# Optimization experiments

Hardware: AMD Instinct MI355X
Metric: run time of the kernel (lower is better)

The kernel has to match this reference:

```python
import jax, jax.numpy as jnp
import numpy as np

B, N, C = 8, 1024, 768
H, D = 12, 64  # num_heads, head_dim; C == H*D
SCALE = 1.0 / np.sqrt(D)
NEG_INF = -1e9


def setup_inputs() -> dict:
    key = jax.random.key(0)
    k1, k2, k3, k4 = jax.random.split(key, 4)
    x = jax.random.normal(k1, (B, N, C), dtype=jnp.float32)
    # additive padding mask: 0 for valid tokens, -1e9 for padded tail
    lengths = jax.random.randint(k2, (B,), N // 2, N + 1)  # valid lengths per sample
    pad = jnp.arange(N)[None, :] >= lengths[:, None]       # [B, N] True = padded
    attn_mask = jnp.where(pad, NEG_INF, 0.0).astype(jnp.float32)[:, None, None, :]  # [B,1,1,N]
    W_qkv = jax.random.normal(k3, (C, 3 * C), dtype=jnp.float32) * (C ** -0.5)
    b_qkv = jnp.zeros((3 * C,), dtype=jnp.float32)
    W_proj = jax.random.normal(k4, (C, C), dtype=jnp.float32) * (C ** -0.5)
    b_proj = jnp.zeros((C,), dtype=jnp.float32)
    return {"x": x, "attn_mask": attn_mask, "W_qkv": W_qkv, "b_qkv": b_qkv,
            "W_proj": W_proj, "b_proj": b_proj}


def reference(x, attn_mask, W_qkv, b_qkv, W_proj, b_proj):
    qkv = (x @ W_qkv + b_qkv).reshape(B, N, 3, H, D)
    qkv = jnp.transpose(qkv, (2, 0, 3, 1, 4))
    q, k, v = qkv[0], qkv[1], qkv[2]
    attn = jnp.einsum('bhnd,bhmd->bhnm', q, k) * SCALE  # [B, H, N, N]
    attn = attn + attn_mask                              # broadcast [B,1,1,N]
    attn = jax.nn.softmax(attn, axis=-1)
    out = jnp.einsum('bhnm,bhmd->bhnd', attn, v)         # [B, H, N, D]
    out = jnp.transpose(out, (0, 2, 1, 3)).reshape(B, N, C)
    return out @ W_proj + b_proj
```

## Files before the change

kernel.cpp:

```cpp
#include <hip/hip_runtime.h>
#include <stdint.h>

#define NB 8
#define NHEAD 12
#define SEQ 1024
#define CDIM 768
#define HDIM 64

#define SCALE_L2E 0.1803368801111244f
#define L2E 1.4426950408889634f

typedef __attribute__((ext_vector_type(8))) short bf16x8;
typedef __attribute__((ext_vector_type(4))) short bf16x4;
typedef __attribute__((ext_vector_type(4))) float f32x4;
typedef __attribute__((ext_vector_type(4))) unsigned short us4;

__device__ __forceinline__ void gload_lds16(const void* g, void* l) {
  __builtin_amdgcn_global_load_lds((const __attribute__((address_space(1))) void*)g,
                                   (__attribute__((address_space(3))) void*)l,
                                   16, 0, 0);
}

__device__ __forceinline__ unsigned short f2bf(float f) {
  __bf16 h = (__bf16)f;
  return __builtin_bit_cast(unsigned short, h);
}

__device__ __forceinline__ f32x4 mfma16(bf16x8 a, bf16x8 b, f32x4 c) {
  return __builtin_amdgcn_mfma_f32_16x16x32_bf16(a, b, c, 0, 0, 0);
}


__global__ void cvt_x_kernel(const float* __restrict__ in,
                             unsigned short* __restrict__ out, int n8) {
  int i = blockIdx.x * blockDim.x + threadIdx.x;
  if (i >= n8) return;
  const float4* p = (const float4*)in;
  float4 a = p[2 * i], b = p[2 * i + 1];
  union { bf16x8 v; unsigned short h[8]; } u;
  u.h[0] = f2bf(a.x); u.h[1] = f2bf(a.y); u.h[2] = f2bf(a.z); u.h[3] = f2bf(a.w);
  u.h[4] = f2bf(b.x); u.h[5] = f2bf(b.y); u.h[6] = f2bf(b.z); u.h[7] = f2bf(b.w);
  ((bf16x8*)out)[i] = u.v;
}

__global__ void tconv_kernel(const float* __restrict__ in,
                             unsigned short* __restrict__ out, int K, int N) {
  __shared__ float tile[32][33];
  int tx = threadIdx.x & 31, ty = threadIdx.x >> 5;
  int n0 = blockIdx.x * 32, k0 = blockIdx.y * 32;
#pragma unroll
  for (int i = 0; i < 4; i++)
    tile[ty + 8 * i][tx] = in[(size_t)(k0 + ty + 8 * i) * N + n0 + tx];
  __syncthreads();
#pragma unroll
  for (int i = 0; i < 4; i++)
    out[(size_t)(n0 + ty + 8 * i) * K + k0 + tx] = f2bf(tile[tx][ty + 8 * i]);
}

template <int EPI>
__global__ __launch_bounds__(256, 4)
void gemm_bt_kernel(const unsigned short* __restrict__ A,
                    const unsigned short* __restrict__ Bt,
                    const float* __restrict__ bias,
                    unsigned short* __restrict__ q_out,
                    unsigned short* __restrict__ k_out,
                    unsigned short* __restrict__ v_out,
                    float* __restrict__ f_out,
                    int M, int N, int K) {
  __shared__ __align__(16) unsigned short As[128 * 64];
  __shared__ __align__(16) unsigned short Bs[128 * 64];
  const int t = threadIdx.x;
  const int w = t >> 6, l = t & 63;
  const int g = l >> 4, lr = l & 15;
  const int wr = w >> 1, wc = w & 1;
  const int nTN = N >> 7;
  const int bpx = gridDim.x >> 3;
  const int orig = (blockIdx.x & 7) * bpx + (blockIdx.x >> 3);
  const int bm = orig / nTN, bn = orig % nTN;
  const int m0 = bm << 7, n0 = bn << 7;

  f32x4 acc[4][4];
#pragma unroll
  for (int i = 0; i < 4; i++)
#pragma unroll
    for (int j = 0; j < 4; j++) acc[i][j] = f32x4{0.f, 0.f, 0.f, 0.f};

  const unsigned short* aP[4];
  const unsigned short* bP[4];
  unsigned short* lA[4];
  unsigned short* lB[4];
#pragma unroll
  for (int i = 0; i < 4; i++) {
    int c = t + 256 * i;
    int r = c >> 3, s = c & 7;
    int ko = (s ^ (r & 7)) * 8;
    aP[i] = A + (size_t)(m0 + r) * K + ko;
    bP[i] = Bt + (size_t)(n0 + r) * K + ko;
    lA[i] = As + c * 8;
    lB[i] = Bs + c * 8;
  }

  for (int kk = 0; kk < K; kk += 64) {
#pragma unroll
    for (int i = 0; i < 4; i++) {
      gload_lds16(aP[i] + kk, lA[i]);
      gload_lds16(bP[i] + kk, lB[i]);
    }
    __syncthreads();
#pragma unroll
    for (int ks = 0; ks < 2; ks++) {
      const int slot = ((ks * 4 + g) ^ (lr & 7)) << 3;
      bf16x8 af[4];
#pragma unroll
      for (int i = 0; i < 4; i++) {
        int row = wr * 64 + i * 16 + lr;
        af[i] = *(const bf16x8*)(As + row * 64 + slot);
      }
#pragma unroll
      for (int j = 0; j < 4; j++) {
        int row = wc * 64 + j * 16 + lr;
        bf16x8 bfr = *(const bf16x8*)(Bs + row * 64 + slot);
#pragma unroll
        for (int i = 0; i < 4; i++) acc[i][j] = mfma16(af[i], bfr, acc[i][j]);
      }
    }
    __syncthreads();
  }

  float bv[4];
#pragma unroll
  for (int j = 0; j < 4; j++) bv[j] = bias[n0 + wc * 64 + j * 16 + lr];

  if (EPI == 1) {
#pragma unroll
    for (int i = 0; i < 4; i++) {
      int mrow = m0 + wr * 64 + i * 16 + 4 * g;
#pragma unroll
      for (int j = 0; j < 4; j++) {
        int n = n0 + wc * 64 + j * 16 + lr;
#pragma unroll
        for (int r = 0; r < 4; r++)
          f_out[(size_t)(mrow + r) * N + n] = acc[i][j][r] + bv[j];
      }
    }
  } else {
    const int which = n0 / CDIM;
    const int bb = m0 / SEQ;
    const int tok0 = (m0 % SEQ) + wr * 64;
#pragma unroll
    for (int j = 0; j < 4; j++) {
      int ncol = (n0 % CDIM) + wc * 64 + j * 16;
      int hh = ncol / 64;
      int d = (ncol % 64) + lr;
#pragma unroll
      for (int i = 0; i < 4; i++) {
        int tokb = tok0 + i * 16 + 4 * g;
        if (which == 2) {
          us4 pk;
#pragma unroll
          for (int r = 0; r < 4; r++) pk[r] = f2bf(acc[i][j][r] + bv[j]);
          *(us4*)(v_out + ((size_t)(bb * NHEAD + hh) * 64 + d) * SEQ + tokb) = pk;
        } else {
          unsigned short* dst = (which == 0) ? q_out : k_out;
#pragma unroll
          for (int r = 0; r < 4; r++)
            dst[((size_t)(bb * NHEAD + hh) * SEQ + tokb + r) * 64 + d] =
                f2bf(acc[i][j][r] + bv[j]);
        }
      }
    }
  }
}

__global__ __launch_bounds__(256, 3)
void attn_kernel(const unsigned short* __restrict__ Qb,
                 const unsigned short* __restrict__ Kb,
                 const unsigned short* __restrict__ Vt,
                 const float* __restrict__ mask,
                 unsigned short* __restrict__ Ob) {
  __shared__ __align__(16) unsigned short Qs[128 * 64];
  __shared__ __align__(16) unsigned short Ks[128 * 64];
  __shared__ __align__(16) unsigned short Vs[64 * 128];
  __shared__ __align__(16) float smask[128];

  const int hwb = blockIdx.x;
  const int x = hwb & 7;
  const int i = hwb >> 3;
  const int qt = i & 7;
  const int bh = (i >> 3) * 8 + x;
  const int h = bh % NHEAD, b = bh / NHEAD;

  const int t = threadIdx.x, w = t >> 6, l = t & 63;
  const int g = l >> 4, lr = l & 15;

  const unsigned short* Qg = Qb + (((size_t)b * NHEAD + h) * SEQ + qt * 128) * 64;
  const unsigned short* Kg = Kb + ((size_t)b * NHEAD + h) * SEQ * 64;
  const unsigned short* Vg = Vt + ((size_t)b * NHEAD + h) * 64 * SEQ;
  const float* mg = mask + (size_t)b * SEQ;

  int nkb = 8;
#pragma unroll
  for (int kb = 7; kb >= 4; kb--)
    if (mg[kb * 128] < -1e8f) nkb = kb;

  bf16x8 kreg[4], vreg[4];
  float mreg;
  auto prefetch = [&](int kb) {
#pragma unroll
    for (int ii = 0; ii < 4; ii++) {
      int c = t + 256 * ii;
      int rk = c >> 3, sk = c & 7;
      kreg[ii] = *(const bf16x8*)(Kg + (size_t)(kb * 128 + rk) * 64 +
                                  ((sk ^ (rk & 7)) << 3));
      int rv = c >> 4, sv = c & 15;
      vreg[ii] = *(const bf16x8*)(Vg + (size_t)rv * SEQ + kb * 128 +
                                  ((sv ^ (rv & 7)) << 3));
    }
    mreg = (t < 128) ? mg[kb * 128 + t] * L2E : 0.f;
  };
  auto commit = [&]() {
#pragma unroll
    for (int ii = 0; ii < 4; ii++) {
      *(bf16x8*)(Ks + (t + 256 * ii) * 8) = kreg[ii];
      *(bf16x8*)(Vs + (t + 256 * ii) * 8) = vreg[ii];
    }
    if (t < 128) smask[t] = mreg;
  };

#pragma unroll
  for (int ii = 0; ii < 4; ii++) {
    int c = t + 256 * ii;
    int row = c >> 3, sl = c & 7;
    gload_lds16(Qg + row * 64 + ((sl ^ (row & 7)) << 3), Qs + c * 8);
  }
  prefetch(0);
  __syncthreads();

  bf16x8 qfr[2][2];
#pragma unroll
  for (int qi = 0; qi < 2; qi++)
#pragma unroll
    for (int ks = 0; ks < 2; ks++) {
      int row = w * 32 + qi * 16 + lr;
      qfr[qi][ks] =
          *(const bf16x8*)(Qs + row * 64 + (((ks * 4 + g) ^ (lr & 7)) << 3));
    }

  float l_run[2] = {0.f, 0.f};
  f32x4 oacc[2][4];
#pragma unroll
  for (int qi = 0; qi < 2; qi++)
#pragma unroll
    for (int df = 0; df < 4; df++) oacc[qi][df] = f32x4{0.f, 0.f, 0.f, 0.f};

  for (int kb = 0; kb < nkb; kb++) {
    __syncthreads();
    commit();
    __syncthreads();
    if (kb + 1 < nkb) prefetch(kb + 1);

    float bs[2] = {0.f, 0.f};
    bf16x8 pa[4][2];
#pragma unroll
    for (int kc = 0; kc < 4; kc++) {
      f32x4 s0[2], s1[2];
#pragma unroll
      for (int qi = 0; qi < 2; qi++) {
        s0[qi] = f32x4{0.f, 0.f, 0.f, 0.f};
        s1[qi] = f32x4{0.f, 0.f, 0.f, 0.f};
      }
#pragma unroll
      for (int ks = 0; ks < 2; ks++) {
        int row0 = (2 * kc) * 16 + lr;
        int row1 = (2 * kc + 1) * 16 + lr;
        int slot = ((ks * 4 + g) ^ (lr & 7)) << 3;
        bf16x8 a0 = *(const bf16x8*)(Ks + row0 * 64 + slot);
        bf16x8 a1 = *(const bf16x8*)(Ks + row1 * 64 + slot);
        s0[0] = mfma16(a0, qfr[0][ks], s0[0]);
        s0[1] = mfma16(a0, qfr[1][ks], s0[1]);
        s1[0] = mfma16(a1, qfr[0][ks], s1[0]);
        s1[1] = mfma16(a1, qfr[1][ks], s1[1]);
      }
      f32x4 mv0 = *(const f32x4*)(smask + (2 * kc) * 16 + 4 * g);
      f32x4 mv1 = *(const f32x4*)(smask + (2 * kc + 1) * 16 + 4 * g);
#pragma unroll
      for (int qi = 0; qi < 2; qi++) {
        union { bf16x8 v; unsigned short hh[8]; } u;
#pragma unroll
        for (int r = 0; r < 4; r++) {
          float p0 = __builtin_amdgcn_exp2f(fmaf(s0[qi][r], SCALE_L2E, mv0[r]));
          float p1 = __builtin_amdgcn_exp2f(fmaf(s1[qi][r], SCALE_L2E, mv1[r]));
          bs[qi] += p0 + p1;
          u.hh[r] = f2bf(p0);
          u.hh[4 + r] = f2bf(p1);
        }
        pa[kc][qi] = u.v;
      }
    }
    bs[0] += __shfl_xor(bs[0], 16);
    bs[0] += __shfl_xor(bs[0], 32);
    bs[1] += __shfl_xor(bs[1], 16);
    bs[1] += __shfl_xor(bs[1], 32);
    l_run[0] += bs[0];
    l_run[1] += bs[1];

    const int sw = (lr & 7) << 4;
#pragma unroll
    for (int kc = 0; kc < 4; kc++) {
#pragma unroll
      for (int df = 0; df < 4; df++) {
        const char* vp = (const char*)(Vs + (df * 16 + lr) * 128);
        bf16x4 lo = *(const bf16x4*)(vp + ((kc * 64 + 8 * g) ^ sw));
        bf16x4 hi = *(const bf16x4*)(vp + ((kc * 64 + 32 + 8 * g) ^ sw));
        bf16x8 vb = __builtin_shufflevector(lo, hi, 0, 1, 2, 3, 4, 5, 6, 7);
        oacc[0][df] = mfma16(pa[kc][0], vb, oacc[0][df]);
        oacc[1][df] = mfma16(pa[kc][1], vb, oacc[1][df]);
      }
    }
  }

#pragma unroll
  for (int qi = 0; qi < 2; qi++) {
    float linv = 1.f / l_run[qi];
#pragma unroll
    for (int r = 0; r < 4; r++) {
      float li = __shfl(linv, 4 * g + r);
      int tok = qt * 128 + w * 32 + qi * 16 + 4 * g + r;
#pragma unroll
      for (int df = 0; df < 4; df++) {
        float val = oacc[qi][df][r] * li;
        Ob[((size_t)b * SEQ + tok) * CDIM + h * 64 + df * 16 + lr] = f2bf(val);
      }
    }
  }
}

extern "C" void kernel_launch(void* const* d_in, const int* in_sizes, int n_in,
                              void* d_out, int out_size, void* d_ws,
                              size_t ws_size, hipStream_t stream) {
  const float* x = (const float*)d_in[0];
  const float* mask = (const float*)d_in[1];
  const float* Wqkv = (const float*)d_in[2];
  const float* bqkv = (const float*)d_in[3];
  const float* Wproj = (const float*)d_in[4];
  const float* bproj = (const float*)d_in[5];
  float* out = (float*)d_out;

  char* ws = (char*)d_ws;
  size_t off = 0;
  auto take = [&](size_t bytes) {
    char* p = ws + off;
    off += (bytes + 255) & ~(size_t)255;
    return p;
  };
  unsigned short* xb = (unsigned short*)take((size_t)NB * SEQ * CDIM * 2);
  unsigned short* wqt = (unsigned short*)take((size_t)3 * CDIM * CDIM * 2);
  unsigned short* wpt = (unsigned short*)take((size_t)CDIM * CDIM * 2);
  unsigned short* Qb = (unsigned short*)take((size_t)NB * NHEAD * SEQ * 64 * 2);
  unsigned short* Kbf = (unsigned short*)take((size_t)NB * NHEAD * SEQ * 64 * 2);
  unsigned short* Vt = (unsigned short*)take((size_t)NB * NHEAD * SEQ * 64 * 2);
  unsigned short* Ob = (unsigned short*)take((size_t)NB * SEQ * CDIM * 2);

  int n8 = NB * SEQ * CDIM / 8;
  cvt_x_kernel<<<(n8 + 255) / 256, 256, 0, stream>>>(x, xb, n8);
  tconv_kernel<<<dim3(3 * CDIM / 32, CDIM / 32), 256, 0, stream>>>(Wqkv, wqt,
                                                                   CDIM, 3 * CDIM);
  tconv_kernel<<<dim3(CDIM / 32, CDIM / 32), 256, 0, stream>>>(Wproj, wpt, CDIM,
                                                               CDIM);
  gemm_bt_kernel<0><<<(NB * SEQ / 128) * (3 * CDIM / 128), 256, 0, stream>>>(
      xb, wqt, bqkv, Qb, Kbf, Vt, nullptr, NB * SEQ, 3 * CDIM, CDIM);
  attn_kernel<<<NB * NHEAD * 8, 256, 0, stream>>>(Qb, Kbf, Vt, mask, Ob);
  gemm_bt_kernel<1><<<(NB * SEQ / 128) * (CDIM / 128), 256, 0, stream>>>(
      Ob, wpt, bproj, nullptr, nullptr, nullptr, out, NB * SEQ, CDIM, CDIM);
}
```

Before: 199.0 us.

## Template GEMM tiles, register-prefetch next K slab, use smaller tiles for output projection

Turns the GEMM tile size into template parameters and replaces the direct global-to-LDS loads with a register prefetch. The next K slab is loaded into registers while the current slab is being computed, then written to LDS. The output-projection GEMM now uses 64x64 tiles, which gives 4x more blocks, to improve occupancy and CU fill for the smaller N=768 problem. The cost is extra register pressure and an extra VGPR-to-LDS write step.

New measurement: 214.9 us. +8.0%, slower.

```diff
diff --git a/kernel.cpp b/kernel.cpp
--- a/kernel.cpp
+++ b/kernel.cpp
@@ -57,7 +57,7 @@
     out[(size_t)(n0 + ty + 8 * i) * K + k0 + tx] = f2bf(tile[tx][ty + 8 * i]);
 }
 
-template <int EPI>
+template <int BM, int BN, int EPI>
 __global__ __launch_bounds__(256, 4)
 void gemm_bt_kernel(const unsigned short* __restrict__ A,
                     const unsigned short* __restrict__ Bt,
@@ -67,77 +67,90 @@
                     unsigned short* __restrict__ v_out,
                     float* __restrict__ f_out,
                     int M, int N, int K) {
-  __shared__ __align__(16) unsigned short As[128 * 64];
-  __shared__ __align__(16) unsigned short Bs[128 * 64];
+  constexpr int WM = BM / 2, WN = BN / 2;
+  constexpr int MI = WM / 16, NJ = WN / 16;
+  constexpr int CA = BM / 32, CB = BN / 32;
+  __shared__ __align__(16) unsigned short As[BM * 64];
+  __shared__ __align__(16) unsigned short Bs[BN * 64];
   const int t = threadIdx.x;
   const int w = t >> 6, l = t & 63;
   const int g = l >> 4, lr = l & 15;
   const int wr = w >> 1, wc = w & 1;
-  const int nTN = N >> 7;
+  const int nTN = N / BN;
   const int bpx = gridDim.x >> 3;
   const int orig = (blockIdx.x & 7) * bpx + (blockIdx.x >> 3);
   const int bm = orig / nTN, bn = orig % nTN;
-  const int m0 = bm << 7, n0 = bn << 7;
-
-  f32x4 acc[4][4];
-#pragma unroll
-  for (int i = 0; i < 4; i++)
-#pragma unroll
-    for (int j = 0; j < 4; j++) acc[i][j] = f32x4{0.f, 0.f, 0.f, 0.f};
-
-  const unsigned short* aP[4];
-  const unsigned short* bP[4];
-  unsigned short* lA[4];
-  unsigned short* lB[4];
-#pragma unroll
-  for (int i = 0; i < 4; i++) {
-    int c = t + 256 * i;
-    int r = c >> 3, s = c & 7;
-    int ko = (s ^ (r & 7)) * 8;
-    aP[i] = A + (size_t)(m0 + r) * K + ko;
-    bP[i] = Bt + (size_t)(n0 + r) * K + ko;
-    lA[i] = As + c * 8;
-    lB[i] = Bs + c * 8;
-  }
-
+  const int m0 = bm * BM, n0 = bn * BN;
+
+  f32x4 acc[MI][NJ];
+#pragma unroll
+  for (int i = 0; i < MI; i++)
+#pragma unroll
+    for (int j = 0; j < NJ; j++) acc[i][j] = f32x4{0.f, 0.f, 0.f, 0.f};
+
+  const unsigned short* aP[CA];
+  const unsigned short* bP[CB];
+#pragma unroll
+  for (int i = 0; i < CA; i++) {
+    int c = t + 256 * i, r = c >> 3, s = c & 7;
+    aP[i] = A + (size_t)(m0 + r) * K + (s ^ (r & 7)) * 8;
+  }
+#pragma unroll
+  for (int i = 0; i < CB; i++) {
+    int c = t + 256 * i, r = c >> 3, s = c & 7;
+    bP[i] = Bt + (size_t)(n0 + r) * K + (s ^ (r & 7)) * 8;
+  }
+
+  bf16x8 areg[CA], breg[CB];
+  auto prefetch = [&](int kk) {
+#pragma unroll
+    for (int i = 0; i < CA; i++) areg[i] = *(const bf16x8*)(aP[i] + kk);
+#pragma unroll
+    for (int i = 0; i < CB; i++) breg[i] = *(const bf16x8*)(bP[i] + kk);
+  };
+  auto commit = [&]() {
+#pragma unroll
+    for (int i = 0; i < CA; i++) *(bf16x8*)(As + (t + 256 * i) * 8) = areg[i];
+#pragma unroll
+    for (int i = 0; i < CB; i++) *(bf16x8*)(Bs + (t + 256 * i) * 8) = breg[i];
+  };
+
+  prefetch(0);
   for (int kk = 0; kk < K; kk += 64) {
-#pragma unroll
-    for (int i = 0; i < 4; i++) {
-      gload_lds16(aP[i] + kk, lA[i]);
-      gload_lds16(bP[i] + kk, lB[i]);
-    }
+    commit();
     __syncthreads();
+    if (kk + 64 < K) prefetch(kk + 64);
 #pragma unroll
     for (int ks = 0; ks < 2; ks++) {
       const int slot = ((ks * 4 + g) ^ (lr & 7)) << 3;
-      bf16x8 af[4];
-#pragma unroll
-      for (int i = 0; i < 4; i++) {
-        int row = wr * 64 + i * 16 + lr;
+      bf16x8 af[MI];
+#pragma unroll
+      for (int i = 0; i < MI; i++) {
+        int row = wr * WM + i * 16 + lr;
         af[i] = *(const bf16x8*)(As + row * 64 + slot);
       }
 #pragma unroll
-      for (int j = 0; j < 4; j++) {
-        int row = wc * 64 + j * 16 + lr;
+      for (int j = 0; j < NJ; j++) {
+        int row = wc * WN + j * 16 + lr;
         bf16x8 bfr = *(const bf16x8*)(Bs + row * 64 + slot);
 #pragma unroll
-        for (int i = 0; i < 4; i++) acc[i][j] = mfma16(af[i], bfr, acc[i][j]);
+        for (int i = 0; i < MI; i++) acc[i][j] = mfma16(af[i], bfr, acc[i][j]);
       }
     }
     __syncthreads();
   }
 
-  float bv[4];
-#pragma unroll
-  for (int j = 0; j < 4; j++) bv[j] = bias[n0 + wc * 64 + j * 16 + lr];
+  float bv[NJ];
+#pragma unroll
+  for (int j = 0; j < NJ; j++) bv[j] = bias[n0 + wc * WN + j * 16 + lr];
 
   if (EPI == 1) {
 #pragma unroll
-    for (int i = 0; i < 4; i++) {
-      int mrow = m0 + wr * 64 + i * 16 + 4 * g;
-#pragma unroll
-      for (int j = 0; j < 4; j++) {
-        int n = n0 + wc * 64 + j * 16 + lr;
+    for (int i = 0; i < MI; i++) {
+      int mrow = m0 + wr * WM + i * 16 + 4 * g;
+#pragma unroll
+      for (int j = 0; j < NJ; j++) {
+        int n = n0 + wc * WN + j * 16 + lr;
 #pragma unroll
         for (int r = 0; r < 4; r++)
           f_out[(size_t)(mrow + r) * N + n] = acc[i][j][r] + bv[j];
@@ -146,14 +159,14 @@
   } else {
     const int which = n0 / CDIM;
     const int bb = m0 / SEQ;
-    const int tok0 = (m0 % SEQ) + wr * 64;
-#pragma unroll
-    for (int j = 0; j < 4; j++) {
-      int ncol = (n0 % CDIM) + wc * 64 + j * 16;
+    const int tok0 = (m0 % SEQ) + wr * WM;
+#pragma unroll
+    for (int j = 0; j < NJ; j++) {
+      int ncol = (n0 % CDIM) + wc * WN + j * 16;
       int hh = ncol / 64;
       int d = (ncol % 64) + lr;
 #pragma unroll
-      for (int i = 0; i < 4; i++) {
+      for (int i = 0; i < MI; i++) {
         int tokb = tok0 + i * 16 + 4 * g;
         if (which == 2) {
           us4 pk;
@@ -367,9 +380,11 @@
                                                                    CDIM, 3 * CDIM);
   tconv_kernel<<<dim3(CDIM / 32, CDIM / 32), 256, 0, stream>>>(Wproj, wpt, CDIM,
                                                                CDIM);
-  gemm_bt_kernel<0><<<(NB * SEQ / 128) * (3 * CDIM / 128), 256, 0, stream>>>(
-      xb, wqt, bqkv, Qb, Kbf, Vt, nullptr, NB * SEQ, 3 * CDIM, CDIM);
+  gemm_bt_kernel<128, 128, 0>
+      <<<(NB * SEQ / 128) * (3 * CDIM / 128), 256, 0, stream>>>(
+          xb, wqt, bqkv, Qb, Kbf, Vt, nullptr, NB * SEQ, 3 * CDIM, CDIM);
   attn_kernel<<<NB * NHEAD * 8, 256, 0, stream>>>(Qb, Kbf, Vt, mask, Ob);
-  gemm_bt_kernel<1><<<(NB * SEQ / 128) * (CDIM / 128), 256, 0, stream>>>(
-      Ob, wpt, bproj, nullptr, nullptr, nullptr, out, NB * SEQ, CDIM, CDIM);
-}
+  gemm_bt_kernel<64, 64, 1>
+      <<<(NB * SEQ / 64) * (CDIM / 64), 256, 0, stream>>>(
+          Ob, wpt, bproj, nullptr, nullptr, nullptr, out, NB * SEQ, CDIM, CDIM);
+}
```
